# Kernel tuning notes

Measured on AMD Instinct MI355X. Metric: run time of the kernel, lower is better.

## Reference

```python
import jax, jax.numpy as jnp
import numpy as np

N_POINTS = 2_000_000
NUM_GRAPHS = 16384
HID = 40  # ffn_param hidden_layer_size
SLOPE = 0.01  # torch default LeakyReLU negative slope


def _w(key, fan_in, fan_out):
    return jax.random.normal(key, (fan_in, fan_out), dtype=jnp.float32) / np.sqrt(fan_in)


def ffn(x, W1, W2, final_linear=False):
    # FFN with n_layers=2, bias=False, hidden=40; dropout is identity in eval.
    h = jax.nn.leaky_relu(x @ W1, SLOPE)
    h = h @ W2
    return h if final_linear else jax.nn.leaky_relu(h, SLOPE)


def setup_inputs() -> dict:
    key = jax.random.key(0)
    ks = jax.random.split(key, 10)
    x = jax.random.normal(ks[0], (N_POINTS, 3), dtype=jnp.float32)
    batch = jnp.sort(jax.random.randint(ks[1], (N_POINTS,), 0, NUM_GRAPHS)).astype(jnp.int64)
    return {
        "x": x,
        "batch": batch,
        # EPiC emb_nn: FFN(3 -> 5)
        "W_emb1": _w(ks[2], 3, HID), "W_emb2": _w(ks[3], HID, 5),
        # EPiC global_nn: FFN(5 -> 4)
        "W_glob1": _w(ks[4], 5, HID), "W_glob2": _w(ks[5], HID, 4),
        # EPiC out_nn: FFN(5+4 -> 32)
        "W_out1": _w(ks[6], 9, HID), "W_out2": _w(ks[7], HID, 32),
        # disc: FFN(32 -> 1, final_linear=True)
        "W_disc1": _w(ks[8], 32, HID), "W_disc2": _w(ks[9], HID, 1),
    }


def reference(x, batch, W_emb1, W_emb2, W_glob1, W_glob2, W_out1, W_out2, W_disc1, W_disc2):
    # EPiC block
    xe = ffn(x, W_emb1, W_emb2)                                   # [N, 5]
    x_aggr = jax.ops.segment_sum(xe, batch, num_segments=NUM_GRAPHS,
                                 indices_are_sorted=True)          # [B, 5]
    x_global = ffn(x_aggr, W_glob1, W_glob2)                       # [B, 4]
    xo = ffn(jnp.concatenate([xe, x_global[batch]], axis=-1),
             W_out1, W_out2)                                       # [N, 32]
    # global pool + final discriminator head
    pooled = jax.ops.segment_sum(xo, batch, num_segments=NUM_GRAPHS,
                                 indices_are_sorted=True)          # [B, 32]
    return ffn(pooled, W_disc1, W_disc2, final_linear=True)        # [B, 1]
```

## Files before the change

kernel.cpp:

```cpp
#include <hip/hip_runtime.h>
#include <hip/hip_bf16.h>

#define N_POINTS   2000000
#define NUM_GRAPHS 16384
#define HID        40
#define SLOPE      0.01f

#define TILE_A     512
#define NT_A       ((N_POINTS + TILE_A - 1) / TILE_A)
#define XESA       584

#define TILE       256
#define NTILES     ((N_POINTS + TILE - 1) / TILE)
#define AROW       20
#define XOS        260

typedef __attribute__((ext_vector_type(8))) short short8;
typedef __attribute__((ext_vector_type(4))) float fx4;

__device__ __forceinline__ float lrelu(float v) { return v > 0.f ? v : SLOPE * v; }
__device__ __forceinline__ int padidx(int p) { return p + ((p >> 5) << 2); }
__device__ __forceinline__ unsigned short f2bf(float f) {
    __hip_bfloat16 h = __float2bfloat16(f);
    return *(unsigned short*)&h;
}
__device__ __forceinline__ float bf2f(unsigned short u) {
    unsigned int v = ((unsigned int)u) << 16;
    return __uint_as_float(v);
}

__global__ __launch_bounds__(256, 2) void k_emb_aggr(
    const float* __restrict__ x, const int* __restrict__ batch,
    const float* __restrict__ We1, const float* __restrict__ We2,
    float* __restrict__ x_aggr, unsigned short* __restrict__ xe_out, int use_xe)
{
    __shared__ __align__(16) float sWe1[3 * HID];
    __shared__ __align__(16) float sWe2T[5 * HID];
    __shared__ __align__(16) float xeT[5 * XESA];
    __shared__ __align__(16) int   sbp[XESA];

    int tid = threadIdx.x;
    for (int k = tid; k < 3 * HID; k += 256) sWe1[k] = We1[k];
    for (int k = tid; k < 5 * HID; k += 256) sWe2T[k] = We2[(k % HID) * 5 + k / HID];
    __syncthreads();

    int base = blockIdx.x * TILE_A;
    int p0 = base + tid, p1 = base + 256 + tid;
    bool v0 = p0 < N_POINTS, v1 = p1 < N_POINTS;
    int i0 = v0 ? p0 : (N_POINTS - 1), i1 = v1 ? p1 : (N_POINTS - 1);
    float a0 = x[i0 * 3 + 0], a1 = x[i0 * 3 + 1], a2 = x[i0 * 3 + 2];
    float c0 = x[i1 * 3 + 0], c1 = x[i1 * 3 + 1], c2 = x[i1 * 3 + 2];
    int b0 = v0 ? batch[i0] : -1;
    int b1 = v1 ? batch[i1] : -1;
    sbp[padidx(tid)] = b0;
    sbp[padidx(256 + tid)] = b1;

    float h0[HID], h1[HID];
    const float4* W1r = (const float4*)sWe1;
#pragma unroll
    for (int j4 = 0; j4 < HID / 4; ++j4) {
        float4 wa = W1r[j4], wb = W1r[10 + j4], wc = W1r[20 + j4];
        float wav[4] = {wa.x, wa.y, wa.z, wa.w};
        float wbv[4] = {wb.x, wb.y, wb.z, wb.w};
        float wcv[4] = {wc.x, wc.y, wc.z, wc.w};
#pragma unroll
        for (int k = 0; k < 4; ++k) {
            int j = j4 * 4 + k;
            h0[j] = lrelu(a0 * wav[k] + a1 * wbv[k] + a2 * wcv[k]);
            h1[j] = lrelu(c0 * wav[k] + c1 * wbv[k] + c2 * wcv[k]);
        }
    }

#pragma unroll
    for (int c = 0; c < 5; ++c) {
        const float4* wr = (const float4*)&sWe2T[c * HID];
        float s0 = 0.f, s1 = 0.f;
#pragma unroll
        for (int j4 = 0; j4 < HID / 4; ++j4) {
            float4 w = wr[j4];
            float wv[4] = {w.x, w.y, w.z, w.w};
#pragma unroll
            for (int k = 0; k < 4; ++k) {
                s0 += h0[j4 * 4 + k] * wv[k];
                s1 += h1[j4 * 4 + k] * wv[k];
            }
        }
        float e0 = v0 ? lrelu(s0) : 0.f;
        float e1 = v1 ? lrelu(s1) : 0.f;
        xeT[c * XESA + padidx(tid)] = e0;
        xeT[c * XESA + padidx(256 + tid)] = e1;
        if (use_xe) {
            if (v0) xe_out[(size_t)c * N_POINTS + p0] = f2bf(e0);
            if (v1) xe_out[(size_t)c * N_POINTS + p1] = f2bf(e1);
        }
    }
    __syncthreads();

    if (tid < 80) {
        int ch = tid >> 4, chunk = tid & 15;
        float acc = 0.f;
        int cur = sbp[chunk * 36];
#pragma unroll
        for (int g = 0; g < 8; ++g) {
            float4 v4 = *(const float4*)&xeT[ch * XESA + chunk * 36 + g * 4];
            int4   n4 = *(const int4*)&sbp[chunk * 36 + g * 4];
            float vv[4] = {v4.x, v4.y, v4.z, v4.w};
            int   nn[4] = {n4.x, n4.y, n4.z, n4.w};
#pragma unroll
            for (int k = 0; k < 4; ++k) {
                if (nn[k] != cur) {
                    if (cur >= 0) atomicAdd(&x_aggr[cur * 5 + ch], acc);
                    cur = nn[k];
                    acc = vv[k];
                } else {
                    acc += vv[k];
                }
            }
        }
        if (cur >= 0) atomicAdd(&x_aggr[cur * 5 + ch], acc);
    }
}

__global__ __launch_bounds__(256) void k_global(
    const float* __restrict__ x_aggr,
    const float* __restrict__ Wg1, const float* __restrict__ Wg2,
    const float* __restrict__ Wo1,
    float* __restrict__ g_contrib)
{
    __shared__ float sWg1[5 * HID];
    __shared__ float sWg2[HID * 4];
    __shared__ float sWo1g[4 * HID];
    for (int k = threadIdx.x; k < 5 * HID; k += 256) sWg1[k] = Wg1[k];
    for (int k = threadIdx.x; k < HID * 4; k += 256) sWg2[k] = Wg2[k];
    for (int k = threadIdx.x; k < 4 * HID; k += 256) sWo1g[k] = Wo1[5 * HID + k];
    __syncthreads();

    int bg = blockIdx.x * 256 + threadIdx.x;
    if (bg >= NUM_GRAPHS) return;

    float a[5];
#pragma unroll
    for (int c = 0; c < 5; ++c) a[c] = x_aggr[bg * 5 + c];

    float h[HID];
#pragma unroll
    for (int j = 0; j < HID; ++j) {
        float s = 0.f;
#pragma unroll
        for (int c = 0; c < 5; ++c) s += a[c] * sWg1[c * HID + j];
        h[j] = lrelu(s);
    }
    float g[4];
#pragma unroll
    for (int c = 0; c < 4; ++c) {
        float s = 0.f;
#pragma unroll
        for (int j = 0; j < HID; ++j) s += h[j] * sWg2[j * 4 + c];
        g[c] = lrelu(s);
    }
#pragma unroll
    for (int j = 0; j < HID; ++j) {
        float s = 0.f;
#pragma unroll
        for (int c = 0; c < 4; ++c) s += g[c] * sWo1g[c * HID + j];
        g_contrib[bg * HID + j] = s;
    }
}

__global__ __launch_bounds__(256, 4) void k_out_pool(
    const float* __restrict__ x, const int* __restrict__ batch,
    const float* __restrict__ We1, const float* __restrict__ We2,
    const float* __restrict__ Wo1, const float* __restrict__ Wo2,
    const float* __restrict__ g_contrib,
    const unsigned short* __restrict__ xe_in, int use_xe,
    float* __restrict__ pooled)
{
    __shared__ __align__(16) unsigned int uLds[32 * XOS];
    __shared__ __align__(16) int sb[TILE];
    __shared__ float sWe1[3 * HID];
    __shared__ float sWe2T[5 * HID];
    __shared__ float sWo1[5 * HID];

    int tid = threadIdx.x;
    for (int k = tid; k < 3 * HID; k += 256) sWe1[k] = We1[k];
    for (int k = tid; k < 5 * HID; k += 256) sWe2T[k] = We2[(k % HID) * 5 + k / HID];
    for (int k = tid; k < 5 * HID; k += 256) sWo1[k] = Wo1[k];

    int lane = tid & 63;
    int l16 = lane & 15, quad = lane >> 4;

    short8 bfrag[2][2];
#pragma unroll
    for (int nt = 0; nt < 2; ++nt) {
#pragma unroll
        for (int ks = 0; ks < 2; ++ks) {
#pragma unroll
            for (int j = 0; j < 8; ++j) {
                int kk = ks * 32 + quad * 8 + j;
                float w = (kk < HID) ? Wo2[kk * 32 + nt * 16 + l16] : 0.f;
                bfrag[nt][ks][j] = (short)f2bf(w);
            }
        }
    }
    short8 zfrag = {0, 0, 0, 0, 0, 0, 0, 0};
    __syncthreads();

    for (int t = blockIdx.x; t < NTILES; t += gridDim.x) {
        int i = t * TILE + tid;
        bool v = i < N_POINTS;
        int ic = v ? i : (N_POINTS - 1);
        int b = v ? batch[ic] : -1;
        sb[tid] = b;

        float xe[5];
        if (use_xe) {
#pragma unroll
            for (int c = 0; c < 5; ++c) xe[c] = bf2f(xe_in[(size_t)c * N_POINTS + ic]);
        } else {
            float x0 = x[ic * 3 + 0], x1 = x[ic * 3 + 1], x2 = x[ic * 3 + 2];
            float h[HID];
            const float4* W1r = (const float4*)sWe1;
#pragma unroll
            for (int j4 = 0; j4 < HID / 4; ++j4) {
                float4 wa = W1r[j4], wb = W1r[10 + j4], wc = W1r[20 + j4];
                float wav[4] = {wa.x, wa.y, wa.z, wa.w};
                float wbv[4] = {wb.x, wb.y, wb.z, wb.w};
                float wcv[4] = {wc.x, wc.y, wc.z, wc.w};
#pragma unroll
                for (int k = 0; k < 4; ++k)
                    h[j4 * 4 + k] = lrelu(x0 * wav[k] + x1 * wbv[k] + x2 * wcv[k]);
            }
#pragma unroll
            for (int c = 0; c < 5; ++c) {
                const float4* wr = (const float4*)&sWe2T[c * HID];
                float s = 0.f;
#pragma unroll
                for (int j4 = 0; j4 < HID / 4; ++j4) {
                    float4 w = wr[j4];
                    s += h[j4 * 4 + 0] * w.x + h[j4 * 4 + 1] * w.y + h[j4 * 4 + 2] * w.z + h[j4 * 4 + 3] * w.w;
                }
                xe[c] = lrelu(s);
            }
        }

        const float4* gc4 = (const float4*)(g_contrib + (size_t)(v ? b : 0) * HID);
        unsigned int* row = &uLds[tid * AROW];
#pragma unroll
        for (int j4 = 0; j4 < HID / 4; ++j4) {
            float4 g = gc4[j4];
            float sv[4] = {g.x, g.y, g.z, g.w};
#pragma unroll
            for (int c = 0; c < 5; ++c) {
                float4 w = ((const float4*)&sWo1[c * HID])[j4];
                float wvv[4] = {w.x, w.y, w.z, w.w};
#pragma unroll
                for (int k = 0; k < 4; ++k) sv[k] += xe[c] * wvv[k];
            }
            __hip_bfloat162 q0 = __float22bfloat162_rn(make_float2(lrelu(sv[0]), lrelu(sv[1])));
            __hip_bfloat162 q1 = __float22bfloat162_rn(make_float2(lrelu(sv[2]), lrelu(sv[3])));
            uint2 u;
            u.x = *(unsigned int*)&q0; u.y = *(unsigned int*)&q1;
            *(uint2*)(row + j4 * 2) = u;
        }

        fx4 xov[4][2];
#pragma unroll
        for (int m = 0; m < 4; ++m) {
            int mt = (tid >> 6) * 4 + m;
            const unsigned int* arow = &uLds[(mt * 16 + l16) * AROW];
            short8 a0 = *(const short8*)(arow + quad * 4);
            short8 a1 = (quad == 0) ? *(const short8*)(arow + 16) : zfrag;
#pragma unroll
            for (int nt = 0; nt < 2; ++nt) {
                fx4 acc = {0.f, 0.f, 0.f, 0.f};
                acc = __builtin_amdgcn_mfma_f32_16x16x32_bf16(a0, bfrag[nt][0], acc, 0, 0, 0);
                acc = __builtin_amdgcn_mfma_f32_16x16x32_bf16(a1, bfrag[nt][1], acc, 0, 0, 0);
#pragma unroll
                for (int r = 0; r < 4; ++r) acc[r] = lrelu(acc[r]);
                xov[m][nt] = acc;
            }
        }
        __syncthreads();

        float* xoT = (float*)uLds;
#pragma unroll
        for (int m = 0; m < 4; ++m) {
            int mt = (tid >> 6) * 4 + m;
#pragma unroll
            for (int nt = 0; nt < 2; ++nt) {
                int ch = nt * 16 + l16;
                int pt = mt * 16 + quad * 4;
                *(fx4*)&xoT[ch * XOS + pt] = xov[m][nt];
            }
        }
        __syncthreads();

        {
            int ch = tid & 31, chunk = tid >> 5;
            float acc = 0.f;
            int cur = sb[chunk * 32];
#pragma unroll
            for (int g = 0; g < 8; ++g) {
                float4 v4 = *(const float4*)&xoT[ch * XOS + chunk * 32 + g * 4];
                int4   n4 = *(const int4*)&sb[chunk * 32 + g * 4];
                float vv[4] = {v4.x, v4.y, v4.z, v4.w};
                int   nn[4] = {n4.x, n4.y, n4.z, n4.w};
#pragma unroll
                for (int k = 0; k < 4; ++k) {
                    if (nn[k] != cur) {
                        if (cur >= 0) atomicAdd(&pooled[cur * 32 + ch], acc);
                        cur = nn[k];
                        acc = vv[k];
                    } else {
                        acc += vv[k];
                    }
                }
            }
            if (cur >= 0) atomicAdd(&pooled[cur * 32 + ch], acc);
        }
        __syncthreads();
    }
}

__global__ __launch_bounds__(256) void k_disc(
    const float* __restrict__ pooled,
    const float* __restrict__ Wd1, const float* __restrict__ Wd2,
    float* __restrict__ out)
{
    __shared__ float sWd1T[HID * 32];
    __shared__ float sWd2[HID];
    for (int k = threadIdx.x; k < 32 * HID; k += 256) sWd1T[k] = Wd1[(k % 32) * HID + k / 32];
    for (int k = threadIdx.x; k < HID; k += 256) sWd2[k] = Wd2[k];
    __syncthreads();

    int bg = blockIdx.x * 256 + threadIdx.x;
    if (bg >= NUM_GRAPHS) return;

    float p[32];
    const float4* pp = (const float4*)(pooled + (size_t)bg * 32);
#pragma unroll
    for (int c4 = 0; c4 < 8; ++c4) {
        float4 vv = pp[c4];
        p[c4 * 4 + 0] = vv.x; p[c4 * 4 + 1] = vv.y; p[c4 * 4 + 2] = vv.z; p[c4 * 4 + 3] = vv.w;
    }

    float acc = 0.f;
#pragma unroll
    for (int j = 0; j < HID; ++j) {
        const float4* wr = (const float4*)&sWd1T[j * 32];
        float s = 0.f;
#pragma unroll
        for (int c4 = 0; c4 < 8; ++c4) {
            float4 w = wr[c4];
            s += p[c4 * 4 + 0] * w.x + p[c4 * 4 + 1] * w.y + p[c4 * 4 + 2] * w.z + p[c4 * 4 + 3] * w.w;
        }
        acc += lrelu(s) * sWd2[j];
    }
    out[bg] = acc;
}

extern "C" void kernel_launch(void* const* d_in, const int* in_sizes, int n_in,
                              void* d_out, int out_size, void* d_ws, size_t ws_size,
                              hipStream_t stream) {
    const float* x     = (const float*)d_in[0];
    const int*   batch = (const int*)  d_in[1];
    const float* We1   = (const float*)d_in[2];
    const float* We2   = (const float*)d_in[3];
    const float* Wg1   = (const float*)d_in[4];
    const float* Wg2   = (const float*)d_in[5];
    const float* Wo1   = (const float*)d_in[6];
    const float* Wo2   = (const float*)d_in[7];
    const float* Wd1   = (const float*)d_in[8];
    const float* Wd2   = (const float*)d_in[9];
    float* out = (float*)d_out;

    float* x_aggr    = (float*)d_ws;
    float* pooled    = x_aggr + NUM_GRAPHS * 5;
    float* g_contrib = pooled + NUM_GRAPHS * 32;
    size_t head_bytes = (size_t)NUM_GRAPHS * (5 + 32 + HID) * sizeof(float);
    unsigned short* xe_ws = (unsigned short*)((char*)d_ws + head_bytes);
    size_t need = head_bytes + (size_t)N_POINTS * 5 * sizeof(unsigned short);
    int use_xe = (ws_size >= need) ? 1 : 0;

    hipMemsetAsync(d_ws, 0, (size_t)NUM_GRAPHS * (5 + 32) * sizeof(float), stream);

    int gblk = (NUM_GRAPHS + 255) / 256;
    k_emb_aggr<<<NT_A, 256, 0, stream>>>(x, batch, We1, We2, x_aggr, xe_ws, use_xe);
    k_global <<<gblk, 256, 0, stream>>>(x_aggr, Wg1, Wg2, Wo1, g_contrib);
    k_out_pool<<<1024, 256, 0, stream>>>(x, batch, We1, We2, Wo1, Wo2, g_contrib,
                                         xe_ws, use_xe, pooled);
    k_disc   <<<gblk, 256, 0, stream>>>(pooled, Wd1, Wd2, out);
}
```

Baseline: 191.2 us.

## Make out-pool LDS staging per-wave and shrink emb tile to one point per thread

```diff
diff --git a/kernel.cpp b/kernel.cpp
--- a/kernel.cpp
+++ b/kernel.cpp
@@ -6,14 +6,15 @@
 #define HID        40
 #define SLOPE      0.01f
 
-#define TILE_A     512
+#define TILE_A     256
 #define NT_A       ((N_POINTS + TILE_A - 1) / TILE_A)
-#define XESA       584
+#define XESA       288
 
 #define TILE       256
 #define NTILES     ((N_POINTS + TILE - 1) / TILE)
 #define AROW       20
-#define XOS        260
+#define XOS        68
+#define WREG       (32 * XOS)
 
 typedef __attribute__((ext_vector_type(8))) short short8;
 typedef __attribute__((ext_vector_type(4))) float fx4;
@@ -29,7 +30,7 @@
     return __uint_as_float(v);
 }
 
-__global__ __launch_bounds__(256, 2) void k_emb_aggr(
+__global__ __launch_bounds__(256, 4) void k_emb_aggr(
     const float* __restrict__ x, const int* __restrict__ batch,
     const float* __restrict__ We1, const float* __restrict__ We2,
     float* __restrict__ x_aggr, unsigned short* __restrict__ xe_out, int use_xe)
@@ -44,18 +45,14 @@
     for (int k = tid; k < 5 * HID; k += 256) sWe2T[k] = We2[(k % HID) * 5 + k / HID];
     __syncthreads();
 
-    int base = blockIdx.x * TILE_A;
-    int p0 = base + tid, p1 = base + 256 + tid;
-    bool v0 = p0 < N_POINTS, v1 = p1 < N_POINTS;
-    int i0 = v0 ? p0 : (N_POINTS - 1), i1 = v1 ? p1 : (N_POINTS - 1);
-    float a0 = x[i0 * 3 + 0], a1 = x[i0 * 3 + 1], a2 = x[i0 * 3 + 2];
-    float c0 = x[i1 * 3 + 0], c1 = x[i1 * 3 + 1], c2 = x[i1 * 3 + 2];
-    int b0 = v0 ? batch[i0] : -1;
-    int b1 = v1 ? batch[i1] : -1;
-    sbp[padidx(tid)] = b0;
-    sbp[padidx(256 + tid)] = b1;
-
-    float h0[HID], h1[HID];
+    int p = blockIdx.x * TILE_A + tid;
+    bool v = p < N_POINTS;
+    int ic = v ? p : (N_POINTS - 1);
+    float x0 = x[ic * 3 + 0], x1 = x[ic * 3 + 1], x2 = x[ic * 3 + 2];
+    int b = v ? batch[ic] : -1;
+    sbp[padidx(tid)] = b;
+
+    float h[HID];
     const float4* W1r = (const float4*)sWe1;
 #pragma unroll
     for (int j4 = 0; j4 < HID / 4; ++j4) {
@@ -64,40 +61,27 @@
         float wbv[4] = {wb.x, wb.y, wb.z, wb.w};
         float wcv[4] = {wc.x, wc.y, wc.z, wc.w};
 #pragma unroll
-        for (int k = 0; k < 4; ++k) {
-            int j = j4 * 4 + k;
-            h0[j] = lrelu(a0 * wav[k] + a1 * wbv[k] + a2 * wcv[k]);
-            h1[j] = lrelu(c0 * wav[k] + c1 * wbv[k] + c2 * wcv[k]);
-        }
+        for (int k = 0; k < 4; ++k)
+            h[j4 * 4 + k] = lrelu(x0 * wav[k] + x1 * wbv[k] + x2 * wcv[k]);
     }
 
 #pragma unroll
     for (int c = 0; c < 5; ++c) {
         const float4* wr = (const float4*)&sWe2T[c * HID];
-        float s0 = 0.f, s1 = 0.f;
+        float s = 0.f;
 #pragma unroll
         for (int j4 = 0; j4 < HID / 4; ++j4) {
             float4 w = wr[j4];
-            float wv[4] = {w.x, w.y, w.z, w.w};
-#pragma unroll
-            for (int k = 0; k < 4; ++k) {
-                s0 += h0[j4 * 4 + k] * wv[k];
-                s1 += h1[j4 * 4 + k] * wv[k];
-            }
-        }
-        float e0 = v0 ? lrelu(s0) : 0.f;
-        float e1 = v1 ? lrelu(s1) : 0.f;
-        xeT[c * XESA + padidx(tid)] = e0;
-        xeT[c * XESA + padidx(256 + tid)] = e1;
-        if (use_xe) {
-            if (v0) xe_out[(size_t)c * N_POINTS + p0] = f2bf(e0);
-            if (v1) xe_out[(size_t)c * N_POINTS + p1] = f2bf(e1);
-        }
-    }
-    __syncthreads();
-
-    if (tid < 80) {
-        int ch = tid >> 4, chunk = tid & 15;
+            s += h[j4 * 4 + 0] * w.x + h[j4 * 4 + 1] * w.y + h[j4 * 4 + 2] * w.z + h[j4 * 4 + 3] * w.w;
+        }
+        float e = v ? lrelu(s) : 0.f;
+        xeT[c * XESA + padidx(tid)] = e;
+        if (use_xe && v) xe_out[(size_t)c * N_POINTS + p] = f2bf(e);
+    }
+    __syncthreads();
+
+    if (tid < 40) {
+        int ch = tid >> 3, chunk = tid & 7;
         float acc = 0.f;
         int cur = sbp[chunk * 36];
 #pragma unroll
@@ -175,7 +159,7 @@
     const unsigned short* __restrict__ xe_in, int use_xe,
     float* __restrict__ pooled)
 {
-    __shared__ __align__(16) unsigned int uLds[32 * XOS];
+    __shared__ __align__(16) unsigned int uLds[4 * WREG];
     __shared__ __align__(16) int sb[TILE];
     __shared__ float sWe1[3 * HID];
     __shared__ float sWe2T[5 * HID];
@@ -186,8 +170,9 @@
     for (int k = tid; k < 5 * HID; k += 256) sWe2T[k] = We2[(k % HID) * 5 + k / HID];
     for (int k = tid; k < 5 * HID; k += 256) sWo1[k] = Wo1[k];
 
-    int lane = tid & 63;
+    int wid = tid >> 6, lane = tid & 63;
     int l16 = lane & 15, quad = lane >> 4;
+    unsigned int* wreg = &uLds[wid * WREG];
 
     short8 bfrag[2][2];
 #pragma unroll
@@ -243,8 +228,8 @@
             }
         }
 
-        const float4* gc4 = (const float4*)(g_contrib + (size_t)(v ? b : 0) * HID);
-        unsigned int* row = &uLds[tid * AROW];
+        const float4* gc4 = (const float4*)(g_contrib + (size_t)(b >= 0 ? b : 0) * HID);
+        unsigned int* row = &wreg[lane * AROW];
 #pragma unroll
         for (int j4 = 0; j4 < HID / 4; ++j4) {
             float4 g = gc4[j4];
@@ -266,8 +251,7 @@
         fx4 xov[4][2];
 #pragma unroll
         for (int m = 0; m < 4; ++m) {
-            int mt = (tid >> 6) * 4 + m;
-            const unsigned int* arow = &uLds[(mt * 16 + l16) * AROW];
+            const unsigned int* arow = &wreg[(m * 16 + l16) * AROW];
             short8 a0 = *(const short8*)(arow + quad * 4);
             short8 a1 = (quad == 0) ? *(const short8*)(arow + 16) : zfrag;
 #pragma unroll
@@ -280,29 +264,27 @@
                 xov[m][nt] = acc;
             }
         }
-        __syncthreads();
-
-        float* xoT = (float*)uLds;
+
+        float* xoT = (float*)wreg;
 #pragma unroll
         for (int m = 0; m < 4; ++m) {
-            int mt = (tid >> 6) * 4 + m;
 #pragma unroll
             for (int nt = 0; nt < 2; ++nt) {
                 int ch = nt * 16 + l16;
-                int pt = mt * 16 + quad * 4;
-                *(fx4*)&xoT[ch * XOS + pt] = xov[m][nt];
-            }
-        }
-        __syncthreads();
+                *(fx4*)&xoT[ch * XOS + m * 16 + quad * 4] = xov[m][nt];
+            }
+        }
 
         {
-            int ch = tid & 31, chunk = tid >> 5;
+            int ch = lane & 31, half = lane >> 5;
+            int pbase = half * 32;
+            const int* sbw = &sb[wid * 64];
             float acc = 0.f;
-            int cur = sb[chunk * 32];
+            int cur = sbw[pbase];
 #pragma unroll
             for (int g = 0; g < 8; ++g) {
-                float4 v4 = *(const float4*)&xoT[ch * XOS + chunk * 32 + g * 4];
-                int4   n4 = *(const int4*)&sb[chunk * 32 + g * 4];
+                float4 v4 = *(const float4*)&xoT[ch * XOS + pbase + g * 4];
+                int4   n4 = *(const int4*)&sbw[pbase + g * 4];
                 float vv[4] = {v4.x, v4.y, v4.z, v4.w};
                 int   nn[4] = {n4.x, n4.y, n4.z, n4.w};
 #pragma unroll
@@ -318,6 +300,7 @@
             }
             if (cur >= 0) atomicAdd(&pooled[cur * 32 + ch], acc);
         }
+
         __syncthreads();
     }
 }
```

Result: no change. 189.7 us (-0.8%).
